# Performance work log

Hardware: AMD Instinct MI355X
Metric: run time of the kernel (lower is better)

## Reference

```python
import jax, jax.numpy as jnp
import numpy as np

B, T, D, H, HS = 8, 1024, 512, 8, 64
LN_EPS = 1e-3  # keras LayerNormalization default


def setup_inputs() -> dict:
    key = jax.random.key(0)
    ks = jax.random.split(key, 8)
    w = lambda k, shape: jax.random.normal(k, shape, jnp.float32) * 0.02
    return {
        "x": jax.random.normal(ks[0], (B, T, D), jnp.float32),
        "pos": jax.random.normal(ks[1], (B, T, D), jnp.float32),
        "gamma": jnp.ones((D,), jnp.float32),
        "beta": jnp.zeros((D,), jnp.float32),
        "wq": w(ks[2], (H, D, HS)),
        "wk": w(ks[3], (H, D, HS)),
        "wv": w(ks[4], (H, D, HS)),
        "wpos": w(ks[5], (H, D, HS)),
        "pos_bias_u": jnp.zeros((H, HS), jnp.float32),
        "pos_bias_v": jnp.zeros((H, HS), jnp.float32),
        "wo": w(ks[6], (H, HS, D)),
        "bo": jnp.zeros((D,), jnp.float32),
    }


def _rel_shift(x):
    # Transformer-XL relative shift: [B,H,T,N] -> [B,H,T,N]
    b, h, t, n = x.shape
    x = jnp.pad(x, ((0, 0), (0, 0), (0, 0), (1, 0)))
    x = x.reshape(b, h, n + 1, t)
    return x[:, :, 1:, :].reshape(b, h, t, n)


def reference(x, pos, gamma, beta, wq, wk, wv, wpos, pos_bias_u, pos_bias_v, wo, bo):
    # LayerNorm (pre-norm)
    mu = jnp.mean(x, axis=-1, keepdims=True)
    var = jnp.mean(jnp.square(x - mu), axis=-1, keepdims=True)
    y = (x - mu) * jax.lax.rsqrt(var + LN_EPS) * gamma + beta

    # per-head projections: [B,T,H,HS]
    q = jnp.einsum("bti,hio->btho", y, wq)
    k = jnp.einsum("bti,hio->btho", y, wk)
    v = jnp.einsum("bti,hio->btho", y, wv)
    p = jnp.einsum("bti,hio->btho", pos, wpos)

    # content (ac) and position (bd) scores: [B,H,T,T]
    ac = jnp.einsum("bnho,bmho->bhnm", q + pos_bias_u, k)
    bd = _rel_shift(jnp.einsum("bnho,bmho->bhnm", q + pos_bias_v, p))
    logits = (ac + bd[..., : ac.shape[-1]]) / jnp.sqrt(jnp.float32(HS))

    attn = jax.nn.softmax(logits, axis=-1)  # dropout=0 / inference
    ctx = jnp.einsum("bhnm,bmho->bnho", attn, v)
    out = jnp.einsum("bnhi,hio->bno", ctx, wo) + bo

    # dropout (inference) is identity; residual add
    return x + out
```

## Files before the change

kernel.cpp:

```cpp
#include <hip/hip_runtime.h>
#include <math.h>

#define Bb 8
#define Tt 1024
#define Dd 512
#define Hh 8
#define HSs 64

typedef __attribute__((ext_vector_type(8))) short bf16x8;
typedef __attribute__((ext_vector_type(4))) float f32x4;
typedef __attribute__((ext_vector_type(8))) unsigned short u16x8;

__device__ __forceinline__ unsigned short f2bf(float f) {
  unsigned u = __float_as_uint(f);
  u += 0x7fffu + ((u >> 16) & 1u);
  return (unsigned short)(u >> 16);
}
__device__ __forceinline__ float bf2f(unsigned short s) {
  return __uint_as_float(((unsigned)s) << 16);
}
__device__ __forceinline__ void gload16(const void* g, void* l) {
  __builtin_amdgcn_global_load_lds(
      (const __attribute__((address_space(1))) void*)g,
      (__attribute__((address_space(3))) void*)l, 16, 0, 0);
}

__global__ __launch_bounds__(256) void prep_w(
    const float* __restrict__ wq, const float* __restrict__ wk,
    const float* __restrict__ wv, const float* __restrict__ wpos,
    const float* __restrict__ wo, unsigned short* __restrict__ wt,
    unsigned short* __restrict__ wo_t) {
  __shared__ unsigned short lds[64][65];
  int t = threadIdx.x, blk = blockIdx.x;
  if (blk < 256) {
    int z = blk >> 6, h = (blk >> 3) & 7, dt = blk & 7;
    const float* src = (z == 0) ? wq : (z == 1) ? wk : (z == 2) ? wv : wpos;
    const float* base = src + (size_t)h * 32768 + (size_t)dt * 4096;
#pragma unroll
    for (int p = 0; p < 4; ++p) {
      int idx = p * 1024 + t * 4;
      float4 v = *(const float4*)(base + idx);
      int d = idx >> 6, o = idx & 63;
      lds[o + 0][d] = f2bf(v.x);
      lds[o + 1][d] = f2bf(v.y);
      lds[o + 2][d] = f2bf(v.z);
      lds[o + 3][d] = f2bf(v.w);
    }
    __syncthreads();
    int o = t >> 2, dc = (t & 3) * 16;
    u16x8 w0, w1;
#pragma unroll
    for (int j = 0; j < 8; ++j) { w0[j] = lds[o][dc + j]; w1[j] = lds[o][dc + 8 + j]; }
    unsigned short* dst =
        wt + (size_t)z * 262144 + (size_t)((h << 6) + o) * 512 + dt * 64 + dc;
    *(u16x8*)dst = w0;
    *(u16x8*)(dst + 8) = w1;
  } else {
    int b2 = blk - 256, h = b2 >> 3, dt = b2 & 7;
    const float* base = wo + (size_t)h * 32768 + (size_t)dt * 64;
#pragma unroll
    for (int p = 0; p < 4; ++p) {
      int idx = p * 1024 + t * 4;
      int o = idx >> 6, dl = idx & 63;
      float4 v = *(const float4*)(base + (size_t)o * 512 + dl);
      lds[dl + 0][o] = f2bf(v.x);
      lds[dl + 1][o] = f2bf(v.y);
      lds[dl + 2][o] = f2bf(v.z);
      lds[dl + 3][o] = f2bf(v.w);
    }
    __syncthreads();
    int dl = t >> 2, oc = (t & 3) * 16;
    u16x8 w0, w1;
#pragma unroll
    for (int j = 0; j < 8; ++j) { w0[j] = lds[dl][oc + j]; w1[j] = lds[dl][oc + 8 + j]; }
    unsigned short* dst = wo_t + (size_t)(dt * 64 + dl) * 512 + (h << 6) + oc;
    *(u16x8*)dst = w0;
    *(u16x8*)(dst + 8) = w1;
  }
}

__global__ __launch_bounds__(256) void ln_pos_kernel(
    const float* __restrict__ x, const float* __restrict__ pos,
    const float* __restrict__ gamma, const float* __restrict__ beta,
    unsigned short* __restrict__ y, unsigned short* __restrict__ posb) {
  int wid = threadIdx.x >> 6, lane = threadIdx.x & 63;
  int blk = blockIdx.x;
  if (blk >= 2048) {
    int row = (blk - 2048) * 4 + wid;
    const float* pr = pos + (size_t)row * Dd + lane * 8;
    float4 a = *(const float4*)pr;
    float4 b = *(const float4*)(pr + 4);
    float v[8] = {a.x, a.y, a.z, a.w, b.x, b.y, b.z, b.w};
    u16x8 o8;
#pragma unroll
    for (int j = 0; j < 8; ++j) o8[j] = f2bf(v[j]);
    *(u16x8*)(posb + (size_t)row * Dd + lane * 8) = o8;
    return;
  }
  int row = blk * 4 + wid;
  const float* xr = x + (size_t)row * Dd + lane * 8;
  float4 v0 = *(const float4*)xr;
  float4 v1 = *(const float4*)(xr + 4);
  float xv[8] = {v0.x, v0.y, v0.z, v0.w, v1.x, v1.y, v1.z, v1.w};
  float s = 0.f, ss = 0.f;
#pragma unroll
  for (int j = 0; j < 8; ++j) { s += xv[j]; ss += xv[j] * xv[j]; }
#pragma unroll
  for (int m = 1; m < 64; m <<= 1) {
    s += __shfl_xor(s, m);
    ss += __shfl_xor(ss, m);
  }
  float mu = s * (1.f / 512.f);
  float var = ss * (1.f / 512.f) - mu * mu;
  float inv = rsqrtf(var + 1e-3f);
  const float4 g0 = *(const float4*)(gamma + lane * 8);
  const float4 g1 = *(const float4*)(gamma + lane * 8 + 4);
  const float4 b0 = *(const float4*)(beta + lane * 8);
  const float4 b1 = *(const float4*)(beta + lane * 8 + 4);
  float gv[8] = {g0.x, g0.y, g0.z, g0.w, g1.x, g1.y, g1.z, g1.w};
  float bv[8] = {b0.x, b0.y, b0.z, b0.w, b1.x, b1.y, b1.z, b1.w};
  u16x8 o8;
#pragma unroll
  for (int j = 0; j < 8; ++j)
    o8[j] = f2bf((xv[j] - mu) * inv * gv[j] + bv[j]);
  *(u16x8*)(y + (size_t)row * Dd + lane * 8) = o8;
}

__global__ __launch_bounds__(256) void proj_gemm(
    const unsigned short* __restrict__ y, const unsigned short* __restrict__ posb,
    const unsigned short* __restrict__ wt, unsigned short* __restrict__ q,
    unsigned short* __restrict__ k, unsigned short* __restrict__ v,
    unsigned short* __restrict__ p) {
  __shared__ __align__(16) unsigned short la[2][64 * 32];
  __shared__ __align__(16) unsigned short lb[2][64 * 32];
  int z = blockIdx.z, h = blockIdx.y, m0 = blockIdx.x * 64;
  const unsigned short* A = (z < 3) ? y : posb;
  const unsigned short* Bt = wt + (size_t)z * 262144 + (size_t)h * 64 * 512;
  unsigned short* dst = (z == 0) ? q : (z == 1) ? k : (z == 2) ? v : p;
  int tid = threadIdx.x, wid = tid >> 6, lane = tid & 63;
  int g = lane >> 4, cl = lane & 15;
  int srow = (wid << 4) + (lane >> 2);
  int scsw = (((lane & 3) ^ ((lane >> 3) & 3)) << 3);
  const unsigned short* asrc = A + (size_t)(m0 + srow) * 512 + scsw;
  const unsigned short* bsrc = Bt + (size_t)srow * 512 + scsw;
  int rk = (cl >> 1) & 3;
  int aoff = (16 * wid + cl) * 32 + ((g ^ rk) << 3);
  f32x4 acc[4] = {};
  gload16(asrc, la[0] + (wid << 9));
  gload16(bsrc, lb[0] + (wid << 9));
  __syncthreads();
  for (int ks = 0; ks < 16; ++ks) {
    int cur = ks & 1;
    if (ks < 15) {
      gload16(asrc + (ks + 1) * 32, la[cur ^ 1] + (wid << 9));
      gload16(bsrc + (ks + 1) * 32, lb[cur ^ 1] + (wid << 9));
    }
    bf16x8 af = *(const bf16x8*)&la[cur][aoff];
#pragma unroll
    for (int nt = 0; nt < 4; ++nt) {
      bf16x8 bf = *(const bf16x8*)&lb[cur][(nt * 16 + cl) * 32 + ((g ^ rk) << 3)];
      acc[nt] = __builtin_amdgcn_mfma_f32_16x16x32_bf16(af, bf, acc[nt], 0, 0, 0);
    }
    __syncthreads();
  }
#pragma unroll
  for (int nt = 0; nt < 4; ++nt)
#pragma unroll
    for (int r = 0; r < 4; ++r) {
      int m = m0 + 16 * wid + g * 4 + r;
      int b = m >> 10, t = m & 1023;
      int o = nt * 16 + cl;
      dst[(((size_t)(b * 8 + h)) * 1024 + t) * 64 + o] = f2bf(acc[nt][r]);
    }
}

__global__ __launch_bounds__(256) void bd_gemm(
    const unsigned short* __restrict__ q, const unsigned short* __restrict__ p,
    const float* __restrict__ vbias, unsigned short* __restrict__ bdsh, int bh0) {
  __shared__ __align__(16) unsigned short pl[64 * 64];
  int px = blockIdx.x, bh = bh0 + px, b = bh >> 3, h = bh & 7;
  int r0 = blockIdx.y * 64, c0 = blockIdx.z * 64;
  int tid = threadIdx.x, wid = tid >> 6, lane = tid & 63;
  int g = lane >> 4, cl = lane & 15;
  const unsigned short* qbase =
      q + (((size_t)(b * 8 + h)) * 1024 + r0 + 16 * wid + cl) * 64;
  bf16x8 aq[2];
#pragma unroll
  for (int ks = 0; ks < 2; ++ks) {
    bf16x8 raw = *(const bf16x8*)&qbase[ks * 32 + g * 8];
#pragma unroll
    for (int j = 0; j < 8; ++j) {
      float f = bf2f((unsigned short)raw[j]) + vbias[h * 64 + ks * 32 + g * 8 + j];
      raw[j] = (short)f2bf(f);
    }
    aq[ks] = raw;
  }
  const unsigned short* pbase = p + (((size_t)(b * 8 + h)) * 1024 + c0) * 64;
  {
    int rlo = lane >> 3;
    int scc = ((lane & 7) ^ rlo) << 3;
#pragma unroll
    for (int it = 0; it < 2; ++it) {
      int seg = wid + it * 4;
      gload16(pbase + (size_t)(seg * 8 + rlo) * 64 + scc,
              (char*)pl + (seg << 10));
    }
  }
  __syncthreads();
  f32x4 acc[4] = {};
#pragma unroll
  for (int ks = 0; ks < 2; ++ks)
#pragma unroll
    for (int nt = 0; nt < 4; ++nt) {
      int row = nt * 16 + cl;
      int byte = row * 128 + ((ks * 64 + g * 16) ^ ((row & 7) << 4));
      bf16x8 bf = *(const bf16x8*)((char*)pl + byte);
      acc[nt] = __builtin_amdgcn_mfma_f32_16x16x32_bf16(aq[ks], bf, acc[nt], 0, 0, 0);
    }
  unsigned short* outb = bdsh + (size_t)px * 1048576;
#pragma unroll
  for (int nt = 0; nt < 4; ++nt)
#pragma unroll
    for (int r = 0; r < 4; ++r) {
      int rg = r0 + 16 * wid + g * 4 + r;
      int cg = c0 + nt * 16 + cl;
      bool hi = (cg >= 1023 - rg);
      int drow = hi ? rg : rg - 1;
      int dcol = hi ? (cg + rg - 1023) : (cg + rg + 1);
      if (drow >= 0)
        outb[(size_t)drow * 1024 + dcol] = f2bf(acc[nt][r]);
    }
}

__global__ __launch_bounds__(1024) void bd_diag(unsigned short* __restrict__ bd) {
  int px = blockIdx.x, i = threadIdx.x;
  if (i < 1023)
    bd[(size_t)px * 1048576 + (size_t)i * 1024 + i + 1] = 0;
}

__global__ __launch_bounds__(256) void attn_kernel(
    const unsigned short* __restrict__ q, const unsigned short* __restrict__ kg,
    const unsigned short* __restrict__ vg, const float* __restrict__ ubias,
    const unsigned short* __restrict__ bdsh, unsigned short* __restrict__ ctx,
    int bh0) {
  __shared__ __align__(16) unsigned short kt[2][64 * 64];
  __shared__ __align__(16) unsigned short vt[2][64 * 64];
  __shared__ __align__(16) unsigned short bdt[2][64 * 64];
  __shared__ __align__(16) unsigned short pl[4][16 * 64];
  int px = blockIdx.x, bh = bh0 + px, b = bh >> 3, h = bh & 7;
  int i0 = blockIdx.y * 64;
  int tid = threadIdx.x, wid = tid >> 6, lane = tid & 63;
  int g = lane >> 4, cl = lane & 15;
  size_t bhoff = ((size_t)(b * 8 + h)) * 1024;
  const unsigned short* qbase = q + (bhoff + i0 + 16 * wid + cl) * 64;
  bf16x8 aq[2];
#pragma unroll
  for (int ks = 0; ks < 2; ++ks) {
    bf16x8 raw = *(const bf16x8*)&qbase[ks * 32 + g * 8];
#pragma unroll
    for (int j = 0; j < 8; ++j) {
      float f = (bf2f((unsigned short)raw[j]) + ubias[h * 64 + ks * 32 + g * 8 + j]) * 0.125f;
      raw[j] = (short)f2bf(f);
    }
    aq[ks] = raw;
  }
  f32x4 oacc[4] = {};
  float mrun[4], lrun[4];
#pragma unroll
  for (int r = 0; r < 4; ++r) { mrun[r] = -INFINITY; lrun[r] = 0.f; }
  const unsigned short* bdb = bdsh + (size_t)px * 1048576;
  const unsigned short* kbase = kg + bhoff * 64;
  const unsigned short* vbase = vg + bhoff * 64;
  int rlo = lane >> 3;
  int scc = ((lane & 7) ^ rlo) << 3;
  int kc0 = wid, kc1 = wid + 4;
  int vby0 = lane * 128 + ((kc0 * 16) ^ ((lane & 7) << 4));
  int vby1 = lane * 128 + ((kc1 * 16) ^ ((lane & 7) << 4));

#pragma unroll
  for (int it = 0; it < 2; ++it) {
    int seg = wid + it * 4;
    gload16(kbase + (size_t)(seg * 8 + rlo) * 64 + scc, (char*)kt[0] + (seg << 10));
    gload16(bdb + (size_t)(i0 + seg * 8 + rlo) * 1024 + scc,
            (char*)bdt[0] + (seg << 10));
  }
  {
    u16x8 va, vb;
#pragma unroll
    for (int j = 0; j < 8; ++j) {
      va[j] = vbase[(size_t)(kc0 * 8 + j) * 64 + lane];
      vb[j] = vbase[(size_t)(kc1 * 8 + j) * 64 + lane];
    }
    *(u16x8*)((char*)vt[0] + vby0) = va;
    *(u16x8*)((char*)vt[0] + vby1) = vb;
  }
  __syncthreads();

  for (int jt = 0; jt < 16; ++jt) {
    int cur = jt & 1;
    unsigned short* ktc = kt[cur];
    unsigned short* vtc = vt[cur];
    unsigned short* bdtc = bdt[cur];
    u16x8 nva, nvb;
    if (jt < 15) {
      int j1 = (jt + 1) * 64;
#pragma unroll
      for (int it = 0; it < 2; ++it) {
        int seg = wid + it * 4;
        gload16(kbase + (size_t)(j1 + seg * 8 + rlo) * 64 + scc,
                (char*)kt[cur ^ 1] + (seg << 10));
        gload16(bdb + (size_t)(i0 + seg * 8 + rlo) * 1024 + j1 + scc,
                (char*)bdt[cur ^ 1] + (seg << 10));
      }
#pragma unroll
      for (int j = 0; j < 8; ++j) {
        nva[j] = vbase[(size_t)(j1 + kc0 * 8 + j) * 64 + lane];
        nvb[j] = vbase[(size_t)(j1 + kc1 * 8 + j) * 64 + lane];
      }
    }
    f32x4 sacc[4] = {};
#pragma unroll
    for (int ks = 0; ks < 2; ++ks)
#pragma unroll
      for (int nt = 0; nt < 4; ++nt) {
        int row = nt * 16 + cl;
        bf16x8 bk = *(const bf16x8*)((char*)ktc + row * 128 +
                                     ((ks * 64 + g * 16) ^ ((row & 7) << 4)));
        sacc[nt] = __builtin_amdgcn_mfma_f32_16x16x32_bf16(aq[ks], bk, sacc[nt], 0, 0, 0);
      }
    float pmax[4];
#pragma unroll
    for (int r = 0; r < 4; ++r) pmax[r] = -INFINITY;
#pragma unroll
    for (int nt = 0; nt < 4; ++nt)
#pragma unroll
      for (int r = 0; r < 4; ++r) {
        int row = 16 * wid + g * 4 + r;
        int byte = row * 128 + (((nt * 16 + cl) * 2) ^ ((row & 7) << 4));
        float bdv = bf2f(*(const unsigned short*)((const char*)bdtc + byte));
        float s = fmaf(bdv, 0.125f, sacc[nt][r]);
        sacc[nt][r] = s;
        pmax[r] = fmaxf(pmax[r], s);
      }
#pragma unroll
    for (int r = 0; r < 4; ++r) {
      pmax[r] = fmaxf(pmax[r], __shfl_xor(pmax[r], 1));
      pmax[r] = fmaxf(pmax[r], __shfl_xor(pmax[r], 2));
      pmax[r] = fmaxf(pmax[r], __shfl_xor(pmax[r], 4));
      pmax[r] = fmaxf(pmax[r], __shfl_xor(pmax[r], 8));
    }
    float scl[4], rsum[4];
#pragma unroll
    for (int r = 0; r < 4; ++r) {
      float mn = fmaxf(mrun[r], pmax[r]);
      scl[r] = __expf(mrun[r] - mn);
      mrun[r] = mn;
      rsum[r] = 0.f;
    }
#pragma unroll
    for (int nt = 0; nt < 4; ++nt)
#pragma unroll
      for (int r = 0; r < 4; ++r) {
        float pv = __expf(sacc[nt][r] - mrun[r]);
        sacc[nt][r] = pv;
        rsum[r] += pv;
      }
#pragma unroll
    for (int r = 0; r < 4; ++r) {
      rsum[r] += __shfl_xor(rsum[r], 1);
      rsum[r] += __shfl_xor(rsum[r], 2);
      rsum[r] += __shfl_xor(rsum[r], 4);
      rsum[r] += __shfl_xor(rsum[r], 8);
      lrun[r] = lrun[r] * scl[r] + rsum[r];
    }
#pragma unroll
    for (int ot = 0; ot < 4; ++ot) {
      f32x4 t = oacc[ot];
#pragma unroll
      for (int r = 0; r < 4; ++r) t[r] *= scl[r];
      oacc[ot] = t;
    }
    unsigned short* pw = &pl[wid][0];
#pragma unroll
    for (int nt = 0; nt < 4; ++nt)
#pragma unroll
      for (int r = 0; r < 4; ++r) {
        int row = g * 4 + r, col = nt * 16 + cl;
        *(unsigned short*)((char*)pw + row * 128 +
                           ((col * 2) ^ ((row & 7) << 4))) = f2bf(sacc[nt][r]);
      }
    bf16x8 ap[2];
#pragma unroll
    for (int ks = 0; ks < 2; ++ks)
      ap[ks] = *(const bf16x8*)((char*)pw + cl * 128 +
                                ((ks * 64 + g * 16) ^ ((cl & 7) << 4)));
#pragma unroll
    for (int ks = 0; ks < 2; ++ks)
#pragma unroll
      for (int ot = 0; ot < 4; ++ot) {
        int o = ot * 16 + cl;
        bf16x8 bv = *(const bf16x8*)((char*)vtc + o * 128 +
                                     ((ks * 64 + g * 16) ^ ((o & 7) << 4)));
        oacc[ot] = __builtin_amdgcn_mfma_f32_16x16x32_bf16(ap[ks], bv, oacc[ot], 0, 0, 0);
      }
    if (jt < 15) {
      unsigned short* vtn = vt[cur ^ 1];
      *(u16x8*)((char*)vtn + vby0) = nva;
      *(u16x8*)((char*)vtn + vby1) = nvb;
    }
    __syncthreads();
  }
  float rinv[4];
#pragma unroll
  for (int r = 0; r < 4; ++r) rinv[r] = __builtin_amdgcn_rcpf(lrun[r]);
#pragma unroll
  for (int ot = 0; ot < 4; ++ot)
#pragma unroll
    for (int r = 0; r < 4; ++r) {
      int i = i0 + 16 * wid + g * 4 + r;
      int c = h * 64 + ot * 16 + cl;
      ctx[((size_t)b * 1024 + i) * 512 + c] = f2bf(oacc[ot][r] * rinv[r]);
    }
}

__global__ __launch_bounds__(256) void out_gemm(
    const unsigned short* __restrict__ ctx, const unsigned short* __restrict__ wot,
    const float* __restrict__ x, const float* __restrict__ bo,
    float* __restrict__ out) {
  __shared__ __align__(16) unsigned short la[2][64 * 32];
  __shared__ __align__(16) unsigned short lb[2][64 * 32];
  int n0 = blockIdx.y * 64, m0 = blockIdx.x * 64;
  int tid = threadIdx.x, wid = tid >> 6, lane = tid & 63;
  int g = lane >> 4, cl = lane & 15;
  int srow = (wid << 4) + (lane >> 2);
  int scsw = (((lane & 3) ^ ((lane >> 3) & 3)) << 3);
  const unsigned short* asrc = ctx + (size_t)(m0 + srow) * 512 + scsw;
  const unsigned short* bsrc = wot + (size_t)(n0 + srow) * 512 + scsw;
  int rk = (cl >> 1) & 3;
  int aoff = (16 * wid + cl) * 32 + ((g ^ rk) << 3);
  f32x4 acc[4] = {};
  gload16(asrc, la[0] + (wid << 9));
  gload16(bsrc, lb[0] + (wid << 9));
  __syncthreads();
  for (int ks = 0; ks < 16; ++ks) {
    int cur = ks & 1;
    if (ks < 15) {
      gload16(asrc + (ks + 1) * 32, la[cur ^ 1] + (wid << 9));
      gload16(bsrc + (ks + 1) * 32, lb[cur ^ 1] + (wid << 9));
    }
    bf16x8 af = *(const bf16x8*)&la[cur][aoff];
#pragma unroll
    for (int nt = 0; nt < 4; ++nt) {
      bf16x8 bf = *(const bf16x8*)&lb[cur][(nt * 16 + cl) * 32 + ((g ^ rk) << 3)];
      acc[nt] = __builtin_amdgcn_mfma_f32_16x16x32_bf16(af, bf, acc[nt], 0, 0, 0);
    }
    __syncthreads();
  }
#pragma unroll
  for (int nt = 0; nt < 4; ++nt)
#pragma unroll
    for (int r = 0; r < 4; ++r) {
      int m = m0 + 16 * wid + g * 4 + r;
      int n = n0 + nt * 16 + cl;
      out[(size_t)m * 512 + n] = acc[nt][r] + x[(size_t)m * 512 + n] + bo[n];
    }
}

extern "C" void kernel_launch(void* const* d_in, const int* in_sizes, int n_in,
                              void* d_out, int out_size, void* d_ws, size_t ws_size,
                              hipStream_t stream) {
  const float* x = (const float*)d_in[0];
  const float* pos = (const float*)d_in[1];
  const float* gamma = (const float*)d_in[2];
  const float* beta = (const float*)d_in[3];
  const float* wq = (const float*)d_in[4];
  const float* wk = (const float*)d_in[5];
  const float* wv = (const float*)d_in[6];
  const float* wpos = (const float*)d_in[7];
  const float* pbu = (const float*)d_in[8];
  const float* pbv = (const float*)d_in[9];
  const float* wo = (const float*)d_in[10];
  const float* bo = (const float*)d_in[11];
  float* out = (float*)d_out;
  char* ws = (char*)d_ws;

  unsigned short* y_bf = (unsigned short*)(ws + 0);
  unsigned short* pos_bf = (unsigned short*)(ws + 8388608);
  unsigned short* wt = (unsigned short*)(ws + 16777216);
  unsigned short* wo_t = (unsigned short*)(ws + 18874368);
  unsigned short* qb = (unsigned short*)(ws + 19398656);
  unsigned short* kb = (unsigned short*)(ws + 27787264);
  unsigned short* vb = (unsigned short*)(ws + 36175872);
  unsigned short* pb = (unsigned short*)(ws + 44564480);
  unsigned short* ctx = (unsigned short*)(ws + 52953088);
  unsigned short* bdraw = (unsigned short*)(ws + 61341696);

  prep_w<<<320, 256, 0, stream>>>(wq, wk, wv, wpos, wo, wt, wo_t);
  ln_pos_kernel<<<4096, 256, 0, stream>>>(x, pos, gamma, beta, y_bf, pos_bf);
  proj_gemm<<<dim3(128, 8, 4), 256, 0, stream>>>(y_bf, pos_bf, wt, qb, kb, vb, pb);

  size_t fixed = 61341696;
  size_t per = 2097152;
  int nch = 1;
  if (ws_size > fixed + per) nch = (int)((ws_size - fixed) / per);
  if (nch > 64) nch = 64;
  if (nch < 1) nch = 1;
  bd_diag<<<dim3(nch), 1024, 0, stream>>>(bdraw);
  for (int bh0 = 0; bh0 < 64; bh0 += nch) {
    int c = (64 - bh0 < nch) ? (64 - bh0) : nch;
    bd_gemm<<<dim3(c, 16, 16), 256, 0, stream>>>(qb, pb, pbv, bdraw, bh0);
    attn_kernel<<<dim3(c, 16), 256, 0, stream>>>(qb, kb, vb, pbu, bdraw, ctx, bh0);
  }
  out_gemm<<<dim3(128, 8), 256, 0, stream>>>(ctx, wo_t, x, bo, out);
}
```

Measured before the change: 288.1 us.

## Pre-transpose V and widen attention tiles to 128 query rows with exp2 softmax

A new kernel transposes V into a [bh, o, t] layout so the attention kernel can stream V tiles straight into LDS with async global-to-LDS loads, replacing the strided scalar gathers and register staging. The attention block grows to 512 threads covering 128 query rows, so each K/V tile is reused by twice as many rows. The softmax folds log2(e) into the scale and uses exp2. The cost is an extra pass over V, a larger workspace that shrinks the number of bd chunks that fit, and more LDS per block.

```diff
diff --git a/kernel.cpp b/kernel.cpp
--- a/kernel.cpp
+++ b/kernel.cpp
@@ -174,6 +174,30 @@
     }
 }
 
+__global__ __launch_bounds__(256) void v_transpose(
+    const unsigned short* __restrict__ vb, unsigned short* __restrict__ vtr) {
+  __shared__ unsigned short lds[64][65];
+  int blk = blockIdx.x;
+  int bh = blk >> 4, t0 = (blk & 15) * 64;
+  int tid = threadIdx.x;
+  const unsigned short* src = vb + ((size_t)bh * 1024 + t0) * 64;
+#pragma unroll
+  for (int it = 0; it < 2; ++it) {
+    int row = (tid >> 3) + it * 32, oc = (tid & 7) * 8;
+    u16x8 v = *(const u16x8*)&src[(size_t)row * 64 + oc];
+#pragma unroll
+    for (int j = 0; j < 8; ++j) lds[row][oc + j] = v[j];
+  }
+  __syncthreads();
+  int o = tid >> 2, tc = (tid & 3) * 16;
+  u16x8 w0, w1;
+#pragma unroll
+  for (int j = 0; j < 8; ++j) { w0[j] = lds[tc + j][o]; w1[j] = lds[tc + 8 + j][o]; }
+  unsigned short* dst = vtr + ((size_t)bh * 64 + o) * 1024 + t0 + tc;
+  *(u16x8*)dst = w0;
+  *(u16x8*)(dst + 8) = w1;
+}
+
 __global__ __launch_bounds__(256) void bd_gemm(
     const unsigned short* __restrict__ q, const unsigned short* __restrict__ p,
     const float* __restrict__ vbias, unsigned short* __restrict__ bdsh, int bh0) {
@@ -238,20 +262,21 @@
     bd[(size_t)px * 1048576 + (size_t)i * 1024 + i + 1] = 0;
 }
 
-__global__ __launch_bounds__(256) void attn_kernel(
+#define SCEXP 0.18033688f
+__global__ __launch_bounds__(512) void attn_kernel(
     const unsigned short* __restrict__ q, const unsigned short* __restrict__ kg,
-    const unsigned short* __restrict__ vg, const float* __restrict__ ubias,
+    const unsigned short* __restrict__ vtr, const float* __restrict__ ubias,
     const unsigned short* __restrict__ bdsh, unsigned short* __restrict__ ctx,
     int bh0) {
   __shared__ __align__(16) unsigned short kt[2][64 * 64];
   __shared__ __align__(16) unsigned short vt[2][64 * 64];
-  __shared__ __align__(16) unsigned short bdt[2][64 * 64];
-  __shared__ __align__(16) unsigned short pl[4][16 * 64];
+  __shared__ __align__(16) unsigned short bdt[2][128 * 64];
+  __shared__ __align__(16) unsigned short pl[8][16 * 64];
   int px = blockIdx.x, bh = bh0 + px, b = bh >> 3, h = bh & 7;
-  int i0 = blockIdx.y * 64;
+  int i0 = blockIdx.y * 128;
   int tid = threadIdx.x, wid = tid >> 6, lane = tid & 63;
   int g = lane >> 4, cl = lane & 15;
-  size_t bhoff = ((size_t)(b * 8 + h)) * 1024;
+  size_t bhoff = (size_t)bh * 1024;
   const unsigned short* qbase = q + (bhoff + i0 + 16 * wid + cl) * 64;
   bf16x8 aq[2];
 #pragma unroll
@@ -259,7 +284,7 @@
     bf16x8 raw = *(const bf16x8*)&qbase[ks * 32 + g * 8];
 #pragma unroll
     for (int j = 0; j < 8; ++j) {
-      float f = (bf2f((unsigned short)raw[j]) + ubias[h * 64 + ks * 32 + g * 8 + j]) * 0.125f;
+      float f = (bf2f((unsigned short)raw[j]) + ubias[h * 64 + ks * 32 + g * 8 + j]) * SCEXP;
       raw[j] = (short)f2bf(f);
     }
     aq[ks] = raw;
@@ -270,29 +295,17 @@
   for (int r = 0; r < 4; ++r) { mrun[r] = -INFINITY; lrun[r] = 0.f; }
   const unsigned short* bdb = bdsh + (size_t)px * 1048576;
   const unsigned short* kbase = kg + bhoff * 64;
-  const unsigned short* vbase = vg + bhoff * 64;
+  const unsigned short* vtb = vtr + (size_t)bh * 65536;
   int rlo = lane >> 3;
   int scc = ((lane & 7) ^ rlo) << 3;
-  int kc0 = wid, kc1 = wid + 4;
-  int vby0 = lane * 128 + ((kc0 * 16) ^ ((lane & 7) << 4));
-  int vby1 = lane * 128 + ((kc1 * 16) ^ ((lane & 7) << 4));
-
+
+  gload16(kbase + (size_t)(wid * 8 + rlo) * 64 + scc, (char*)kt[0] + (wid << 10));
+  gload16(vtb + (size_t)(wid * 8 + rlo) * 1024 + scc, (char*)vt[0] + (wid << 10));
 #pragma unroll
   for (int it = 0; it < 2; ++it) {
-    int seg = wid + it * 4;
-    gload16(kbase + (size_t)(seg * 8 + rlo) * 64 + scc, (char*)kt[0] + (seg << 10));
+    int seg = wid + it * 8;
     gload16(bdb + (size_t)(i0 + seg * 8 + rlo) * 1024 + scc,
             (char*)bdt[0] + (seg << 10));
-  }
-  {
-    u16x8 va, vb;
-#pragma unroll
-    for (int j = 0; j < 8; ++j) {
-      va[j] = vbase[(size_t)(kc0 * 8 + j) * 64 + lane];
-      vb[j] = vbase[(size_t)(kc1 * 8 + j) * 64 + lane];
-    }
-    *(u16x8*)((char*)vt[0] + vby0) = va;
-    *(u16x8*)((char*)vt[0] + vby1) = vb;
   }
   __syncthreads();
 
@@ -301,21 +314,17 @@
     unsigned short* ktc = kt[cur];
     unsigned short* vtc = vt[cur];
     unsigned short* bdtc = bdt[cur];
-    u16x8 nva, nvb;
     if (jt < 15) {
       int j1 = (jt + 1) * 64;
+      gload16(kbase + (size_t)(j1 + wid * 8 + rlo) * 64 + scc,
+              (char*)kt[cur ^ 1] + (wid << 10));
+      gload16(vtb + (size_t)(wid * 8 + rlo) * 1024 + j1 + scc,
+              (char*)vt[cur ^ 1] + (wid << 10));
 #pragma unroll
       for (int it = 0; it < 2; ++it) {
-        int seg = wid + it * 4;
-        gload16(kbase + (size_t)(j1 + seg * 8 + rlo) * 64 + scc,
-                (char*)kt[cur ^ 1] + (seg << 10));
+        int seg = wid + it * 8;
         gload16(bdb + (size_t)(i0 + seg * 8 + rlo) * 1024 + j1 + scc,
                 (char*)bdt[cur ^ 1] + (seg << 10));
-      }
-#pragma unroll
-      for (int j = 0; j < 8; ++j) {
-        nva[j] = vbase[(size_t)(j1 + kc0 * 8 + j) * 64 + lane];
-        nvb[j] = vbase[(size_t)(j1 + kc1 * 8 + j) * 64 + lane];
       }
     }
     f32x4 sacc[4] = {};
@@ -338,7 +347,7 @@
         int row = 16 * wid + g * 4 + r;
         int byte = row * 128 + (((nt * 16 + cl) * 2) ^ ((row & 7) << 4));
         float bdv = bf2f(*(const unsigned short*)((const char*)bdtc + byte));
-        float s = fmaf(bdv, 0.125f, sacc[nt][r]);
+        float s = fmaf(bdv, SCEXP, sacc[nt][r]);
         sacc[nt][r] = s;
         pmax[r] = fmaxf(pmax[r], s);
       }
@@ -353,7 +362,7 @@
 #pragma unroll
     for (int r = 0; r < 4; ++r) {
       float mn = fmaxf(mrun[r], pmax[r]);
-      scl[r] = __expf(mrun[r] - mn);
+      scl[r] = __builtin_exp2f(mrun[r] - mn);
       mrun[r] = mn;
       rsum[r] = 0.f;
     }
@@ -361,7 +370,7 @@
     for (int nt = 0; nt < 4; ++nt)
 #pragma unroll
       for (int r = 0; r < 4; ++r) {
-        float pv = __expf(sacc[nt][r] - mrun[r]);
+        float pv = __builtin_exp2f(sacc[nt][r] - mrun[r]);
         sacc[nt][r] = pv;
         rsum[r] += pv;
       }
@@ -403,11 +412,6 @@
                                      ((ks * 64 + g * 16) ^ ((o & 7) << 4)));
         oacc[ot] = __builtin_amdgcn_mfma_f32_16x16x32_bf16(ap[ks], bv, oacc[ot], 0, 0, 0);
       }
-    if (jt < 15) {
-      unsigned short* vtn = vt[cur ^ 1];
-      *(u16x8*)((char*)vtn + vby0) = nva;
-      *(u16x8*)((char*)vtn + vby1) = nvb;
-    }
     __syncthreads();
   }
   float rinv[4];
@@ -493,13 +497,15 @@
   unsigned short* vb = (unsigned short*)(ws + 36175872);
   unsigned short* pb = (unsigned short*)(ws + 44564480);
   unsigned short* ctx = (unsigned short*)(ws + 52953088);
-  unsigned short* bdraw = (unsigned short*)(ws + 61341696);
+  unsigned short* vtrans = (unsigned short*)(ws + 61341696);
+  unsigned short* bdraw = (unsigned short*)(ws + 69730304);
 
   prep_w<<<320, 256, 0, stream>>>(wq, wk, wv, wpos, wo, wt, wo_t);
   ln_pos_kernel<<<4096, 256, 0, stream>>>(x, pos, gamma, beta, y_bf, pos_bf);
   proj_gemm<<<dim3(128, 8, 4), 256, 0, stream>>>(y_bf, pos_bf, wt, qb, kb, vb, pb);
-
-  size_t fixed = 61341696;
+  v_transpose<<<1024, 256, 0, stream>>>(vb, vtrans);
+
+  size_t fixed = 69730304;
   size_t per = 2097152;
   int nch = 1;
   if (ws_size > fixed + per) nch = (int)((ws_size - fixed) / per);
@@ -509,7 +515,7 @@
   for (int bh0 = 0; bh0 < 64; bh0 += nch) {
     int c = (64 - bh0 < nch) ? (64 - bh0) : nch;
     bd_gemm<<<dim3(c, 16, 16), 256, 0, stream>>>(qb, pb, pbv, bdraw, bh0);
-    attn_kernel<<<dim3(c, 16), 256, 0, stream>>>(qb, kb, vb, pbu, bdraw, ctx, bh0);
+    attn_kernel<<<dim3(c, 8), 512, 0, stream>>>(qb, kb, vtrans, pbu, bdraw, ctx, bh0);
   }
   out_gemm<<<dim3(128, 8), 256, 0, stream>>>(ctx, wo_t, x, bo, out);
 }
```

Result: no change. 282.5 us (-1.9%).
